# Optimization experiments

Measured on AMD Instinct MI355X. Metric: run time of the kernel, lower is better.

Reference implementation:

```python
import jax, jax.numpy as jnp
import numpy as np

B = 1024        # number of molecule pairs (batch_don.max()+1)
LMAX = 160      # static pad length per molecule (avg ~64 atoms, 12-sigma safe)
D = 128         # embed_dim
H = 4           # num_heads
HD = D // H     # head_dim
SCALE = HD ** -0.5
LN_EPS = 1e-5


def setup_inputs() -> dict:
    key = jax.random.key(0)
    ks = jax.random.split(key, 16)
    N = 65536
    x_don = jax.random.normal(ks[0], (N, D), jnp.float32)
    x_acc = jax.random.normal(ks[1], (N, D), jnp.float32)
    batch_don = jnp.sort(jax.random.randint(ks[2], (N,), 0, B)).astype(jnp.int32)
    batch_acc = jnp.sort(jax.random.randint(ks[3], (N,), 0, B)).astype(jnp.int32)
    s = 1.0 / np.sqrt(D)
    Wq = jax.random.uniform(ks[4], (D, D), jnp.float32, -s, s)
    bq = jax.random.uniform(ks[5], (D,), jnp.float32, -s, s)
    Wk = jax.random.uniform(ks[6], (D, D), jnp.float32, -s, s)
    bk = jax.random.uniform(ks[7], (D,), jnp.float32, -s, s)
    Wv = jax.random.uniform(ks[8], (D, D), jnp.float32, -s, s)
    bv = jax.random.uniform(ks[9], (D,), jnp.float32, -s, s)
    Wo = jax.random.uniform(ks[10], (D, D), jnp.float32, -s, s)
    bo = jax.random.uniform(ks[11], (D,), jnp.float32, -s, s)
    ln_g = jnp.ones((D,), jnp.float32)
    ln_b = jnp.zeros((D,), jnp.float32)
    return {"x_don": x_don, "x_acc": x_acc, "Wq": Wq, "bq": bq, "Wk": Wk, "bk": bk,
            "Wv": Wv, "bv": bv, "Wo": Wo, "bo": bo, "ln_g": ln_g, "ln_b": ln_b,
            "batch_don": batch_don, "batch_acc": batch_acc}


def _pad_segments(x, batch):
    # sorted segment ids -> padded [B, LMAX, D], valid mask [B, LMAX], per-row pos
    n = x.shape[0]
    counts = jnp.zeros((B,), jnp.int32).at[batch].add(1)
    starts = jnp.concatenate([jnp.zeros((1,), jnp.int32), jnp.cumsum(counts)[:-1]])
    pos = jnp.arange(n, dtype=jnp.int32) - starts[batch]
    padded = jnp.zeros((B, LMAX, x.shape[1]), x.dtype).at[batch, pos].set(x)
    mask = jnp.arange(LMAX, dtype=jnp.int32)[None, :] < counts[:, None]
    return padded, mask, pos


def _layer_norm(x, g, b):
    mu = jnp.mean(x, axis=-1, keepdims=True)
    var = jnp.mean((x - mu) ** 2, axis=-1, keepdims=True)
    return (x - mu) * jax.lax.rsqrt(var + LN_EPS) * g + b


def _cross_attn(q_pad, kv_pad, k_mask, Wq, bq, Wk, bk, Wv, bv, Wo, bo, ln_g, ln_b):
    # q_pad: [B, Lq, D], kv_pad: [B, Lk, D], k_mask: [B, Lk]
    Q = (q_pad @ Wq + bq).reshape(B, LMAX, H, HD)
    K = (kv_pad @ Wk + bk).reshape(B, LMAX, H, HD)
    V = (kv_pad @ Wv + bv).reshape(B, LMAX, H, HD)
    scores = jnp.einsum('bqhd,bkhd->bhqk', Q, K) * SCALE
    scores = jnp.where(k_mask[:, None, None, :], scores, -1e30)
    m = jnp.max(scores, axis=-1, keepdims=True)
    e = jnp.exp(scores - m) * k_mask[:, None, None, :]
    attn = e / jnp.maximum(jnp.sum(e, axis=-1, keepdims=True), 1e-9)
    attended = jnp.einsum('bhqk,bkhd->bqhd', attn, V).reshape(B, LMAX, D)
    attended = attended @ Wo + bo
    # NOTE: the original module uses self.norm_don for BOTH directions (norm_acc unused)
    return _layer_norm(q_pad + attended, ln_g, ln_b)


def reference(x_don, x_acc, Wq, bq, Wk, bk, Wv, bv, Wo, bo, ln_g, ln_b, batch_don, batch_acc):
    don_pad, don_mask, don_pos = _pad_segments(x_don, batch_don)
    acc_pad, acc_mask, acc_pos = _pad_segments(x_acc, batch_acc)
    out_don = _cross_attn(don_pad, acc_pad, acc_mask, Wq, bq, Wk, bk, Wv, bv, Wo, bo, ln_g, ln_b)
    out_acc = _cross_attn(acc_pad, don_pad, don_mask, Wq, bq, Wk, bk, Wv, bv, Wo, bo, ln_g, ln_b)
    x_don_enriched = out_don[batch_don, don_pos]
    x_acc_enriched = out_acc[batch_acc, acc_pos]
    return (x_don_enriched, x_acc_enriched)
```

## Files before the change

kernel.cpp:

```cpp
#include <hip/hip_runtime.h>
#include <hip/hip_bf16.h>
#include <stdint.h>

#define NB 1024
#define LMAX 160
#define DIM 128
#define NH 4
#define HDIM 32
#define ATT_SCALE 0.1767766952966369f
#define LN_EPS 1e-5f
#define VTP 164
#define PSP 40
#define WTP 136

typedef __attribute__((ext_vector_type(8))) short bf16x8;
typedef __attribute__((ext_vector_type(4))) float f32x4;

union U8 { uint2 u[2]; uint4 q; bf16x8 v; };

__device__ __forceinline__ ushort f2bf(float f) {
    uint32_t x = __float_as_uint(f);
    x += 0x7fffu + ((x >> 16) & 1u);
    return (ushort)(x >> 16);
}
__device__ __forceinline__ uint32_t pk2bf(float a, float b) {
    return (uint32_t)f2bf(a) | ((uint32_t)f2bf(b) << 16);
}
__device__ __forceinline__ uint32_t pkcvt(float a, float b) {
    __hip_bfloat162 h = __float22bfloat162_rn(make_float2(a, b));
    return *reinterpret_cast<uint32_t*>(&h);
}

__device__ __forceinline__ void wgbar_noflush() {
    asm volatile("s_waitcnt lgkmcnt(0)" ::: "memory");
    __builtin_amdgcn_s_barrier();
    asm volatile("" ::: "memory");
}

__global__ void setup_kernel(const float* __restrict__ Wq, const float* __restrict__ Wk,
                             const float* __restrict__ Wv, const float* __restrict__ Wo,
                             ushort* __restrict__ wtg,
                             const int* __restrict__ bd, const int* __restrict__ ba,
                             int* __restrict__ starts, int* __restrict__ counts, int N)
{
    int t = blockIdx.x * blockDim.x + threadIdx.x;
    {
        int m = t >> 14;
        int idx = t & 16383;
        int k = idx >> 7, c = idx & 127;
        const float* W = (m == 0) ? Wq : (m == 1) ? Wk : (m == 2) ? Wv : Wo;
        wtg[(m << 14) + c * DIM + k] = f2bf(W[idx]);
    }
    if (t < 2 * NB) {
        int side = t >> 10;
        int b = t & (NB - 1);
        const int* arr = side ? ba : bd;
        int lo = 0, hi = N;
        while (lo < hi) { int mid = (lo + hi) >> 1; if (arr[mid] < b) lo = mid + 1; else hi = mid; }
        int st = lo;
        hi = N;
        while (lo < hi) { int mid = (lo + hi) >> 1; if (arr[mid] < b + 1) lo = mid + 1; else hi = mid; }
        starts[t] = st;
        counts[t] = lo - st;
    }
}

__global__ __launch_bounds__(512) void proj_mfma(
    const float* __restrict__ x_don, const float* __restrict__ x_acc,
    const ushort* __restrict__ wtg,
    const float* __restrict__ bq, const float* __restrict__ bk, const float* __restrict__ bv,
    ushort* __restrict__ qkv, int N)
{
    __shared__ ushort wt[128][WTP];
    const int side = blockIdx.y;
    const float* x = side ? x_acc : x_don;
    const int t = threadIdx.x;
    const int lane = t & 63, wid = t >> 6;
    const int r16 = lane & 15, kg = lane >> 4;
    const int wr0 = blockIdx.x * 128 + wid * 16;

    float4 raw[4][2];
    {
        const float* xr = &x[(size_t)(wr0 + r16) * DIM + kg * 8];
        #pragma unroll
        for (int ks = 0; ks < 4; ++ks) {
            raw[ks][0] = *reinterpret_cast<const float4*>(xr + ks * 32);
            raw[ks][1] = *reinterpret_cast<const float4*>(xr + ks * 32 + 4);
        }
    }
    U8 xb[4];
    #pragma unroll
    for (int ks = 0; ks < 4; ++ks) {
        xb[ks].u[0].x = pk2bf(raw[ks][0].x, raw[ks][0].y);
        xb[ks].u[0].y = pk2bf(raw[ks][0].z, raw[ks][0].w);
        xb[ks].u[1].x = pk2bf(raw[ks][1].x, raw[ks][1].y);
        xb[ks].u[1].y = pk2bf(raw[ks][1].z, raw[ks][1].w);
    }

    for (int w = 0; w < 3; ++w) {
        if (w) wgbar_noflush();
        const ushort* wsrc = wtg + ((size_t)w << 14);
        #pragma unroll
        for (int p = 0; p < 4; ++p) {
            int lin = (p * 512 + t) * 8;
            int c = lin >> 7, k = lin & 127;
            *reinterpret_cast<uint4*>(&wt[c][k]) =
                *reinterpret_cast<const uint4*>(&wsrc[c * DIM + k]);
        }
        wgbar_noflush();

        f32x4 acc[8];
        #pragma unroll
        for (int j = 0; j < 8; ++j) acc[j] = (f32x4){0.f, 0.f, 0.f, 0.f};

        #pragma unroll
        for (int ks = 0; ks < 4; ++ks)
            #pragma unroll
            for (int ct = 0; ct < 8; ++ct) {
                bf16x8 bfr = *reinterpret_cast<const bf16x8*>(
                    &wt[ct * 16 + r16][ks * 32 + kg * 8]);
                acc[ct] = __builtin_amdgcn_mfma_f32_16x16x32_bf16(xb[ks].v, bfr, acc[ct], 0, 0, 0);
            }

        const float* bias = (w == 0) ? bq : (w == 1) ? bk : bv;
        float b8[8];
        #pragma unroll
        for (int ct = 0; ct < 8; ++ct) b8[ct] = bias[ct * 16 + r16];

        wgbar_noflush();

        #pragma unroll
        for (int ct = 0; ct < 8; ++ct)
            #pragma unroll
            for (int j = 0; j < 4; ++j)
                wt[wid * 16 + kg * 4 + j][ct * 16 + r16] = f2bf(acc[ct][j] + b8[ct]);

        ushort* outp = qkv + (size_t)(side * 3 + w) * N * DIM;
        const int lr4 = lane >> 4;
        const int c8 = (lane & 15) * 8;
        #pragma unroll
        for (int ps = 0; ps < 4; ++ps) {
            int lr = ps * 4 + lr4;
            uint4 vv = *reinterpret_cast<const uint4*>(&wt[wid * 16 + lr][c8]);
            *reinterpret_cast<uint4*>(&outp[(size_t)(wr0 + lr) * DIM + c8]) = vv;
        }
    }
}

__global__ __launch_bounds__(256) void attn_mfma(
    ushort* __restrict__ qkv,
    const int* __restrict__ starts, const int* __restrict__ counts, int N)
{
    __shared__ __align__(16) ushort Vt[HDIM][VTP];
    __shared__ __align__(16) ushort Ps[4][16][PSP];
    const int b = blockIdx.x, dir = blockIdx.y;
    const int hcol = blockIdx.z * HDIM;
    const int qside = dir, kside = 1 - dir;
    const int qs = starts[qside * NB + b];
    const int nq = counts[qside * NB + b];
    if (nq == 0) return;
    const int kst = starts[kside * NB + b];
    const int nk = min(counts[kside * NB + b], LMAX);
    ushort* Q = qkv + (size_t)(qside * 3) * N * DIM;
    const ushort* K = qkv + (size_t)(kside * 3 + 1) * N * DIM;
    const ushort* V = qkv + (size_t)(kside * 3 + 2) * N * DIM;
    const int t = threadIdx.x;
    const int lane = t & 63, wid = t >> 6;
    const int r16 = lane & 15, g = lane >> 4;

    const int NCK = (nk + 31) >> 5;
    const int NKP = NCK << 5;
    const int NFULL = nk >> 5;
    const bool tail = (nk & 31) != 0;

    U8 ones;
    ones.q = make_uint4(0x3F803F80u, 0x3F803F80u, 0x3F803F80u, 0x3F803F80u);

    {
        const int krl = t >> 2, c = t & 3;
        for (int base = 0; base < nk; base += 64) {
            int kr = base + krl;
            if (kr < nk) {
                uint4 v4 = *reinterpret_cast<const uint4*>(
                    &V[(size_t)(kst + kr) * DIM + hcol + c * 8]);
                uint32_t vv[4] = {v4.x, v4.y, v4.z, v4.w};
                #pragma unroll
                for (int m2 = 0; m2 < 4; ++m2) {
                    Vt[c * 8 + 2 * m2][kr]     = (ushort)(vv[m2] & 0xffffu);
                    Vt[c * 8 + 2 * m2 + 1][kr] = (ushort)(vv[m2] >> 16);
                }
            }
        }
        int pad = NKP - nk;
        for (int i = t; i < (pad << 5); i += 256) {
            int d = i & 31, col = nk + (i >> 5);
            Vt[d][col] = 0;
        }
    }
    __syncthreads();

    for (int q0 = wid * 16; q0 < nq; q0 += 64) {
        const int rq = qs + min(q0 + r16, nq - 1);
        bf16x8 bQ = *reinterpret_cast<const bf16x8*>(&Q[(size_t)rq * DIM + hcol + g * 8]);

        f32x4 oa0 = {0.f, 0.f, 0.f, 0.f}, oa1 = {0.f, 0.f, 0.f, 0.f};
        f32x4 la  = {0.f, 0.f, 0.f, 0.f};

        for (int ck = 0; ck < NFULL; ++ck) {
            const int k0 = ck * 32;
            bf16x8 aK0 = *reinterpret_cast<const bf16x8*>(
                &K[(size_t)(kst + k0 + r16) * DIM + hcol + g * 8]);
            bf16x8 aK1 = *reinterpret_cast<const bf16x8*>(
                &K[(size_t)(kst + k0 + 16 + r16) * DIM + hcol + g * 8]);
            f32x4 s0 = __builtin_amdgcn_mfma_f32_16x16x32_bf16(
                aK0, bQ, (f32x4){0.f, 0.f, 0.f, 0.f}, 0, 0, 0);
            f32x4 s1 = __builtin_amdgcn_mfma_f32_16x16x32_bf16(
                aK1, bQ, (f32x4){0.f, 0.f, 0.f, 0.f}, 0, 0, 0);

            float e[8];
            #pragma unroll
            for (int j = 0; j < 4; ++j) {
                e[j]     = __expf(s0[j] * ATT_SCALE);
                e[4 + j] = __expf(s1[j] * ATT_SCALE);
            }
            uint2 w0, w1;
            w0.x = pkcvt(e[0], e[1]);
            w0.y = pkcvt(e[2], e[3]);
            w1.x = pkcvt(e[4], e[5]);
            w1.y = pkcvt(e[6], e[7]);
            *reinterpret_cast<uint2*>(&Ps[wid][r16][4 * g]) = w0;
            *reinterpret_cast<uint2*>(&Ps[wid][r16][16 + 4 * g]) = w1;
            bf16x8 bP = *reinterpret_cast<const bf16x8*>(&Ps[wid][r16][g * 8]);

            U8 av0, av1;
            av0.u[0] = *reinterpret_cast<const uint2*>(&Vt[r16][k0 + g * 8]);
            av0.u[1] = *reinterpret_cast<const uint2*>(&Vt[r16][k0 + g * 8 + 4]);
            av1.u[0] = *reinterpret_cast<const uint2*>(&Vt[16 + r16][k0 + g * 8]);
            av1.u[1] = *reinterpret_cast<const uint2*>(&Vt[16 + r16][k0 + g * 8 + 4]);
            oa0 = __builtin_amdgcn_mfma_f32_16x16x32_bf16(av0.v, bP, oa0, 0, 0, 0);
            oa1 = __builtin_amdgcn_mfma_f32_16x16x32_bf16(av1.v, bP, oa1, 0, 0, 0);
            la  = __builtin_amdgcn_mfma_f32_16x16x32_bf16(ones.v, bP, la, 0, 0, 0);
        }

        if (tail) {
            const int k0 = NFULL * 32;
            const int rk0 = kst + min(k0 + r16, nk - 1);
            const int rk1 = kst + min(k0 + 16 + r16, nk - 1);
            bf16x8 aK0 = *reinterpret_cast<const bf16x8*>(&K[(size_t)rk0 * DIM + hcol + g * 8]);
            bf16x8 aK1 = *reinterpret_cast<const bf16x8*>(&K[(size_t)rk1 * DIM + hcol + g * 8]);
            f32x4 s0 = __builtin_amdgcn_mfma_f32_16x16x32_bf16(
                aK0, bQ, (f32x4){0.f, 0.f, 0.f, 0.f}, 0, 0, 0);
            f32x4 s1 = __builtin_amdgcn_mfma_f32_16x16x32_bf16(
                aK1, bQ, (f32x4){0.f, 0.f, 0.f, 0.f}, 0, 0, 0);

            float e[8];
            #pragma unroll
            for (int j = 0; j < 4; ++j) {
                e[j]     = (k0 + 4 * g + j < nk)      ? __expf(s0[j] * ATT_SCALE) : 0.f;
                e[4 + j] = (k0 + 16 + 4 * g + j < nk) ? __expf(s1[j] * ATT_SCALE) : 0.f;
            }
            uint2 w0, w1;
            w0.x = pkcvt(e[0], e[1]);
            w0.y = pkcvt(e[2], e[3]);
            w1.x = pkcvt(e[4], e[5]);
            w1.y = pkcvt(e[6], e[7]);
            *reinterpret_cast<uint2*>(&Ps[wid][r16][4 * g]) = w0;
            *reinterpret_cast<uint2*>(&Ps[wid][r16][16 + 4 * g]) = w1;
            bf16x8 bP = *reinterpret_cast<const bf16x8*>(&Ps[wid][r16][g * 8]);

            U8 av0, av1;
            av0.u[0] = *reinterpret_cast<const uint2*>(&Vt[r16][k0 + g * 8]);
            av0.u[1] = *reinterpret_cast<const uint2*>(&Vt[r16][k0 + g * 8 + 4]);
            av1.u[0] = *reinterpret_cast<const uint2*>(&Vt[16 + r16][k0 + g * 8]);
            av1.u[1] = *reinterpret_cast<const uint2*>(&Vt[16 + r16][k0 + g * 8 + 4]);
            oa0 = __builtin_amdgcn_mfma_f32_16x16x32_bf16(av0.v, bP, oa0, 0, 0, 0);
            oa1 = __builtin_amdgcn_mfma_f32_16x16x32_bf16(av1.v, bP, oa1, 0, 0, 0);
            la  = __builtin_amdgcn_mfma_f32_16x16x32_bf16(ones.v, bP, la, 0, 0, 0);
        }

        if (q0 + r16 < nq) {
            float inv = 1.f / fmaxf(la[0], 1e-9f);
            ushort* dst = &Q[(size_t)(qs + q0 + r16) * DIM + hcol];
            uint2 o0, o1;
            o0.x = pkcvt(oa0[0] * inv, oa0[1] * inv);
            o0.y = pkcvt(oa0[2] * inv, oa0[3] * inv);
            o1.x = pkcvt(oa1[0] * inv, oa1[1] * inv);
            o1.y = pkcvt(oa1[2] * inv, oa1[3] * inv);
            *reinterpret_cast<uint2*>(dst + 4 * g) = o0;
            *reinterpret_cast<uint2*>(dst + 16 + 4 * g) = o1;
        }
    }
}

__global__ __launch_bounds__(256) void out_mfma(
    const ushort* __restrict__ qkv,
    const float* __restrict__ x_don, const float* __restrict__ x_acc,
    const ushort* __restrict__ wtg,
    const float* __restrict__ bo, const float* __restrict__ ln_g, const float* __restrict__ ln_b,
    float* __restrict__ out, int N)
{
    __shared__ ushort wt[128][WTP];
    const int t = threadIdx.x;
    const int lane = t & 63, wid = t >> 6;
    const int r16 = lane & 15, kg = lane >> 4;
    const int r0 = blockIdx.x * 128;
    const int wr0 = r0 + wid * 32;
    const ushort* attb = qkv + (r0 < N ? (size_t)0 : (size_t)2 * N * DIM);
    const float* xresb = (r0 < N) ? x_don : x_acc;
    const int rx0 = (r0 < N) ? wr0 : wr0 - N;

    const ushort* wsrc = wtg + ((size_t)3 << 14);
    #pragma unroll
    for (int p = 0; p < 8; ++p) {
        int lin = (p * 256 + t) * 8;
        int c = lin >> 7, k = lin & 127;
        *reinterpret_cast<uint4*>(&wt[c][k]) =
            *reinterpret_cast<const uint4*>(&wsrc[c * DIM + k]);
    }

    U8 ab[2][4];
    #pragma unroll
    for (int rt = 0; rt < 2; ++rt)
        #pragma unroll
        for (int ks = 0; ks < 4; ++ks)
            ab[rt][ks].q = *reinterpret_cast<const uint4*>(
                &attb[(size_t)(wr0 + rt * 16 + r16) * DIM + ks * 32 + kg * 8]);

    __syncthreads();

    f32x4 acc[2][8];
    #pragma unroll
    for (int i = 0; i < 2; ++i)
        #pragma unroll
        for (int j = 0; j < 8; ++j) acc[i][j] = (f32x4){0.f, 0.f, 0.f, 0.f};

    #pragma unroll
    for (int ks = 0; ks < 4; ++ks)
        #pragma unroll
        for (int ct = 0; ct < 8; ++ct) {
            bf16x8 bfr = *reinterpret_cast<const bf16x8*>(
                &wt[ct * 16 + r16][ks * 32 + kg * 8]);
            acc[0][ct] = __builtin_amdgcn_mfma_f32_16x16x32_bf16(ab[0][ks].v, bfr, acc[0][ct], 0, 0, 0);
            acc[1][ct] = __builtin_amdgcn_mfma_f32_16x16x32_bf16(ab[1][ks].v, bfr, acc[1][ct], 0, 0, 0);
        }

    float bo8[8], g8[8], be8[8];
    #pragma unroll
    for (int ct = 0; ct < 8; ++ct) {
        int c = ct * 16 + r16;
        bo8[ct] = bo[c]; g8[ct] = ln_g[c]; be8[ct] = ln_b[c];
    }

    #pragma unroll
    for (int rt = 0; rt < 2; ++rt) {
        #pragma unroll
        for (int j = 0; j < 4; ++j) {
            int rl = rt * 16 + kg * 4 + j;
            const float* resr = &xresb[(size_t)(rx0 + rl) * DIM];
            float y[8];
            float s = 0.f, ss = 0.f;
            #pragma unroll
            for (int ct = 0; ct < 8; ++ct) {
                float v = acc[rt][ct][j] + bo8[ct] + resr[ct * 16 + r16];
                y[ct] = v; s += v; ss += v * v;
            }
            #pragma unroll
            for (int mk2 = 1; mk2 < 16; mk2 <<= 1) {
                s  += __shfl_xor(s, mk2);
                ss += __shfl_xor(ss, mk2);
            }
            float mu   = s * (1.f / 128.f);
            float var  = ss * (1.f / 128.f) - mu * mu;
            float rinv = rsqrtf(var + LN_EPS);
            #pragma unroll
            for (int ct = 0; ct < 8; ++ct)
                out[(size_t)(wr0 + rl) * DIM + ct * 16 + r16] =
                    (y[ct] - mu) * rinv * g8[ct] + be8[ct];
        }
    }
}

extern "C" void kernel_launch(void* const* d_in, const int* in_sizes, int n_in,
                              void* d_out, int out_size, void* d_ws, size_t ws_size,
                              hipStream_t stream)
{
    const float* x_don = (const float*)d_in[0];
    const float* x_acc = (const float*)d_in[1];
    const float* Wq = (const float*)d_in[2];  const float* bq = (const float*)d_in[3];
    const float* Wk = (const float*)d_in[4];  const float* bk = (const float*)d_in[5];
    const float* Wv = (const float*)d_in[6];  const float* bv = (const float*)d_in[7];
    const float* Wo = (const float*)d_in[8];  const float* bo = (const float*)d_in[9];
    const float* ln_g = (const float*)d_in[10]; const float* ln_b = (const float*)d_in[11];
    const int* batch_don = (const int*)d_in[12];
    const int* batch_acc = (const int*)d_in[13];
    const int N = in_sizes[0] / DIM;
    float* out = (float*)d_out;

    char* ws = (char*)d_ws;
    int* starts = (int*)ws;
    int* counts = starts + 2 * NB;
    ushort* qkv = (ushort*)(ws + 16384);
    ushort* wtg = (ushort*)(ws + 16384 + (size_t)6 * N * DIM * 2);

    setup_kernel<<<256, 256, 0, stream>>>(Wq, Wk, Wv, Wo, wtg,
                                          batch_don, batch_acc, starts, counts, N);

    dim3 gproj(N / 128, 2);
    proj_mfma<<<gproj, 512, 0, stream>>>(x_don, x_acc, wtg, bq, bk, bv, qkv, N);

    dim3 gattn(NB, 2, NH);
    attn_mfma<<<gattn, 256, 0, stream>>>(qkv, starts, counts, N);

    out_mfma<<<(2 * N) / 128, 256, 0, stream>>>(qkv, x_don, x_acc, wtg,
                                                bo, ln_g, ln_b, out, N);
}
```

Before: 115.9 us.

## Map heads to waves in one attention block and fold scale into Q

The attention grid drops its head dimension. Each 256-thread block now handles all four heads, one per wavefront, and walks every query tile instead of splitting query tiles across waves. The whole V block for all 128 columns is transposed into shared memory once per block, instead of once per head. The softmax scale is applied when Q is projected, which removes a multiply before each exp. This cuts the launch count fourfold and removes redundant block setup, but raises shared memory per block and the serial query loop per wave, which may lower occupancy.

```diff
diff --git a/kernel.cpp b/kernel.cpp
--- a/kernel.cpp
+++ b/kernel.cpp
@@ -123,6 +123,7 @@
             }
 
         const float* bias = (w == 0) ? bq : (w == 1) ? bk : bv;
+        const float sc = (w == 0) ? ATT_SCALE : 1.f;
         float b8[8];
         #pragma unroll
         for (int ct = 0; ct < 8; ++ct) b8[ct] = bias[ct * 16 + r16];
@@ -133,7 +134,8 @@
         for (int ct = 0; ct < 8; ++ct)
             #pragma unroll
             for (int j = 0; j < 4; ++j)
-                wt[wid * 16 + kg * 4 + j][ct * 16 + r16] = f2bf(acc[ct][j] + b8[ct]);
+                wt[wid * 16 + kg * 4 + j][ct * 16 + r16] =
+                    f2bf((acc[ct][j] + b8[ct]) * sc);
 
         ushort* outp = qkv + (size_t)(side * 3 + w) * N * DIM;
         const int lr4 = lane >> 4;
@@ -151,10 +153,9 @@
     ushort* __restrict__ qkv,
     const int* __restrict__ starts, const int* __restrict__ counts, int N)
 {
-    __shared__ __align__(16) ushort Vt[HDIM][VTP];
+    __shared__ __align__(16) ushort Vt[128][VTP];
     __shared__ __align__(16) ushort Ps[4][16][PSP];
     const int b = blockIdx.x, dir = blockIdx.y;
-    const int hcol = blockIdx.z * HDIM;
     const int qside = dir, kside = 1 - dir;
     const int qs = starts[qside * NB + b];
     const int nq = counts[qside * NB + b];
@@ -167,6 +168,7 @@
     const int t = threadIdx.x;
     const int lane = t & 63, wid = t >> 6;
     const int r16 = lane & 15, g = lane >> 4;
+    const int hcol = wid * HDIM;
 
     const int NCK = (nk + 31) >> 5;
     const int NKP = NCK << 5;
@@ -177,12 +179,12 @@
     ones.q = make_uint4(0x3F803F80u, 0x3F803F80u, 0x3F803F80u, 0x3F803F80u);
 
     {
-        const int krl = t >> 2, c = t & 3;
-        for (int base = 0; base < nk; base += 64) {
-            int kr = base + krl;
-            if (kr < nk) {
+        for (int kr = lane; kr < nk; kr += 64) {
+            #pragma unroll
+            for (int ii = 0; ii < 4; ++ii) {
+                int c = wid * 4 + ii;
                 uint4 v4 = *reinterpret_cast<const uint4*>(
-                    &V[(size_t)(kst + kr) * DIM + hcol + c * 8]);
+                    &V[(size_t)(kst + kr) * DIM + c * 8]);
                 uint32_t vv[4] = {v4.x, v4.y, v4.z, v4.w};
                 #pragma unroll
                 for (int m2 = 0; m2 < 4; ++m2) {
@@ -192,14 +194,14 @@
             }
         }
         int pad = NKP - nk;
-        for (int i = t; i < (pad << 5); i += 256) {
-            int d = i & 31, col = nk + (i >> 5);
+        for (int i = t; i < (pad << 7); i += 256) {
+            int d = i & 127, col = nk + (i >> 7);
             Vt[d][col] = 0;
         }
     }
     __syncthreads();
 
-    for (int q0 = wid * 16; q0 < nq; q0 += 64) {
+    for (int q0 = 0; q0 < nq; q0 += 16) {
         const int rq = qs + min(q0 + r16, nq - 1);
         bf16x8 bQ = *reinterpret_cast<const bf16x8*>(&Q[(size_t)rq * DIM + hcol + g * 8]);
 
@@ -220,8 +222,8 @@
             float e[8];
             #pragma unroll
             for (int j = 0; j < 4; ++j) {
-                e[j]     = __expf(s0[j] * ATT_SCALE);
-                e[4 + j] = __expf(s1[j] * ATT_SCALE);
+                e[j]     = __expf(s0[j]);
+                e[4 + j] = __expf(s1[j]);
             }
             uint2 w0, w1;
             w0.x = pkcvt(e[0], e[1]);
@@ -233,10 +235,10 @@
             bf16x8 bP = *reinterpret_cast<const bf16x8*>(&Ps[wid][r16][g * 8]);
 
             U8 av0, av1;
-            av0.u[0] = *reinterpret_cast<const uint2*>(&Vt[r16][k0 + g * 8]);
-            av0.u[1] = *reinterpret_cast<const uint2*>(&Vt[r16][k0 + g * 8 + 4]);
-            av1.u[0] = *reinterpret_cast<const uint2*>(&Vt[16 + r16][k0 + g * 8]);
-            av1.u[1] = *reinterpret_cast<const uint2*>(&Vt[16 + r16][k0 + g * 8 + 4]);
+            av0.u[0] = *reinterpret_cast<const uint2*>(&Vt[hcol + r16][k0 + g * 8]);
+            av0.u[1] = *reinterpret_cast<const uint2*>(&Vt[hcol + r16][k0 + g * 8 + 4]);
+            av1.u[0] = *reinterpret_cast<const uint2*>(&Vt[hcol + 16 + r16][k0 + g * 8]);
+            av1.u[1] = *reinterpret_cast<const uint2*>(&Vt[hcol + 16 + r16][k0 + g * 8 + 4]);
             oa0 = __builtin_amdgcn_mfma_f32_16x16x32_bf16(av0.v, bP, oa0, 0, 0, 0);
             oa1 = __builtin_amdgcn_mfma_f32_16x16x32_bf16(av1.v, bP, oa1, 0, 0, 0);
             la  = __builtin_amdgcn_mfma_f32_16x16x32_bf16(ones.v, bP, la, 0, 0, 0);
@@ -256,8 +258,8 @@
             float e[8];
             #pragma unroll
             for (int j = 0; j < 4; ++j) {
-                e[j]     = (k0 + 4 * g + j < nk)      ? __expf(s0[j] * ATT_SCALE) : 0.f;
-                e[4 + j] = (k0 + 16 + 4 * g + j < nk) ? __expf(s1[j] * ATT_SCALE) : 0.f;
+                e[j]     = (k0 + 4 * g + j < nk)      ? __expf(s0[j]) : 0.f;
+                e[4 + j] = (k0 + 16 + 4 * g + j < nk) ? __expf(s1[j]) : 0.f;
             }
             uint2 w0, w1;
             w0.x = pkcvt(e[0], e[1]);
@@ -269,10 +271,10 @@
             bf16x8 bP = *reinterpret_cast<const bf16x8*>(&Ps[wid][r16][g * 8]);
 
             U8 av0, av1;
-            av0.u[0] = *reinterpret_cast<const uint2*>(&Vt[r16][k0 + g * 8]);
-            av0.u[1] = *reinterpret_cast<const uint2*>(&Vt[r16][k0 + g * 8 + 4]);
-            av1.u[0] = *reinterpret_cast<const uint2*>(&Vt[16 + r16][k0 + g * 8]);
-            av1.u[1] = *reinterpret_cast<const uint2*>(&Vt[16 + r16][k0 + g * 8 + 4]);
+            av0.u[0] = *reinterpret_cast<const uint2*>(&Vt[hcol + r16][k0 + g * 8]);
+            av0.u[1] = *reinterpret_cast<const uint2*>(&Vt[hcol + r16][k0 + g * 8 + 4]);
+            av1.u[0] = *reinterpret_cast<const uint2*>(&Vt[hcol + 16 + r16][k0 + g * 8]);
+            av1.u[1] = *reinterpret_cast<const uint2*>(&Vt[hcol + 16 + r16][k0 + g * 8 + 4]);
             oa0 = __builtin_amdgcn_mfma_f32_16x16x32_bf16(av0.v, bP, oa0, 0, 0, 0);
             oa1 = __builtin_amdgcn_mfma_f32_16x16x32_bf16(av1.v, bP, oa1, 0, 0, 0);
             la  = __builtin_amdgcn_mfma_f32_16x16x32_bf16(ones.v, bP, la, 0, 0, 0);
@@ -408,7 +410,7 @@
     dim3 gproj(N / 128, 2);
     proj_mfma<<<gproj, 512, 0, stream>>>(x_don, x_acc, wtg, bq, bk, bv, qkv, N);
 
-    dim3 gattn(NB, 2, NH);
+    dim3 gattn(NB, 2);
     attn_mfma<<<gattn, 256, 0, stream>>>(qkv, starts, counts, N);
 
     out_mfma<<<(2 * N) / 128, 256, 0, stream>>>(qkv, x_don, x_acc, wtg,
```

Result: no change. 118.1 us (+1.9%).
